# Performance work log

Hardware: AMD Instinct MI355X
Metric: run time of the kernel (lower is better)

The kernel has to match this reference:

```python
import jax, jax.numpy as jnp
import numpy as np

B, C, N, K = 1, 64, 65536, 16

def setup_inputs() -> dict:
    key = jax.random.key(0)
    ks = jax.random.split(key, 12)
    s = 0.02
    return {
        "spa": jax.random.normal(ks[0], (B, C, N), jnp.float32),
        "spe": jax.random.normal(ks[1], (B, C, N), jnp.float32),
        "neighbor_indices": jax.random.randint(ks[2], (B, N, K), 0, N, jnp.int64),
        # spa_MHA params (torch Linear weights, shape [out,in])
        "WQ_spa": jax.random.normal(ks[3], (C, C), jnp.float32) * s,
        "WK_spa": jax.random.normal(ks[4], (C, C), jnp.float32) * s,
        "WV_spa": jax.random.normal(ks[5], (C, C), jnp.float32) * s,
        "bV_spa": jnp.zeros((C,), jnp.float32),
        # spe_MHA params
        "WQ_spe": jax.random.normal(ks[6], (C, C), jnp.float32) * s,
        "WK_spe": jax.random.normal(ks[7], (C, C), jnp.float32) * s,
        "WV_spe": jax.random.normal(ks[8], (C, C), jnp.float32) * s,
        "bV_spe": jnp.zeros((C,), jnp.float32),
    }


def _cross_att(q, nb, WQ, WK, WV, bV):
    # q: [B,N,C], nb: [B,N,K,C]
    Q = jnp.einsum('bnc,dc->bnd', q, WQ)            # [B,N,C]
    Kk = jnp.einsum('bnkc,dc->bnkd', nb, WK)        # [B,N,K,C]
    V = jnp.einsum('bnkc,dc->bnkd', nb, WV) + bV    # [B,N,K,C]
    scores = jnp.einsum('bnd,bnkd->bnk', Q, Kk) / np.sqrt(Q.shape[-1]).astype(Q.dtype)
    attn = jax.nn.softmax(scores, axis=-1)          # [B,N,K]
    ctx = jnp.einsum('bnk,bnkd->bnd', attn, V)      # [B,N,C]
    return ctx.transpose(0, 2, 1)                   # [B,C,N]


def reference(spa, spe, neighbor_indices,
              WQ_spa, WK_spa, WV_spa, bV_spa,
              WQ_spe, WK_spe, WV_spe, bV_spe):
    dims = spa.shape[1]
    feature = jnp.concatenate([spa, spe], axis=1)   # [B,2C,N]
    # gather neighbors: [B,2C,N,K]
    nb = jax.vmap(lambda f, idx: f[:, idx])(feature, neighbor_indices)
    feature_q = feature.transpose(0, 2, 1)          # [B,N,2C]
    nb = nb.transpose(0, 2, 3, 1)                   # [B,N,K,2C]
    spa_feat = _cross_att(feature_q[..., :dims], nb[..., dims:],
                          WQ_spa, WK_spa, WV_spa, bV_spa)
    spe_feat = _cross_att(feature_q[..., dims:], nb[..., :dims],
                          WQ_spe, WK_spe, WV_spe, bV_spe)
    fusion = jnp.concatenate([spa_feat, spe_feat], axis=1)  # [B,2C,N]
    return feature + fusion
```

## Files before the change

kernel.cpp:

```cpp
#include <hip/hip_runtime.h>

#define NPTS 65536

__device__ __forceinline__ float bf_lo(unsigned u) { return __uint_as_float(u << 16); }
__device__ __forceinline__ float bf_hi(unsigned u) { return __uint_as_float(u & 0xFFFF0000u); }
__device__ __forceinline__ unsigned short f2bf(float f) {
    unsigned u = __float_as_uint(f);
    return (unsigned short)((u + 0x7FFFu + ((u >> 16) & 1u)) >> 16);
}
__device__ __forceinline__ float bfu(unsigned short us) {
    return __uint_as_float(((unsigned)us) << 16);
}
__device__ __forceinline__ unsigned pktrunc(float a, float b) {
    return (__float_as_uint(a) >> 16) | (__float_as_uint(b) & 0xFFFF0000u);
}
__device__ __forceinline__ void unpack8(uint4 v, float* o) {
    o[0] = bf_lo(v.x); o[1] = bf_hi(v.x); o[2] = bf_lo(v.y); o[3] = bf_hi(v.y);
    o[4] = bf_lo(v.z); o[5] = bf_hi(v.z); o[6] = bf_lo(v.w); o[7] = bf_hi(v.w);
}
#if __has_builtin(__builtin_amdgcn_fdot2_f32_bf16)
typedef __bf16 bf16x2 __attribute__((ext_vector_type(2)));
__device__ __forceinline__ float dot2acc(unsigned a, unsigned b, float c) {
    return __builtin_amdgcn_fdot2_f32_bf16(__builtin_bit_cast(bf16x2, a),
                                           __builtin_bit_cast(bf16x2, b), c, false);
}
#else
__device__ __forceinline__ float dot2acc(unsigned a, unsigned b, float c) {
    return c + bf_lo(a) * bf_lo(b) + bf_hi(a) * bf_hi(b);
}
#endif
#if __has_builtin(__builtin_amdgcn_rcpf)
__device__ __forceinline__ float fastrcp(float x) { return __builtin_amdgcn_rcpf(x); }
#else
__device__ __forceinline__ float fastrcp(float x) { return 1.0f / x; }
#endif

#if __has_builtin(__builtin_amdgcn_cvt_pk_f32_fp8) && __has_builtin(__builtin_amdgcn_cvt_pk_fp8_f32)
#define USE_FP8 1
typedef float floatx2 __attribute__((ext_vector_type(2)));
__device__ __forceinline__ void unpk_fp8_u32(unsigned u, float* o) {
    floatx2 lo = __builtin_amdgcn_cvt_pk_f32_fp8((int)u, false);
    floatx2 hi = __builtin_amdgcn_cvt_pk_f32_fp8((int)u, true);
    o[0] = lo[0]; o[1] = lo[1]; o[2] = hi[0]; o[3] = hi[1];
}
__device__ __forceinline__ unsigned pk_fp8_4(float a, float b, float c, float d) {
    int v = __builtin_amdgcn_cvt_pk_fp8_f32(a, b, 0, false);
    v = __builtin_amdgcn_cvt_pk_fp8_f32(c, d, v, true);
    return (unsigned)v;
}
#else
#define USE_FP8 0
#endif

typedef __attribute__((ext_vector_type(8))) short short8;
typedef __attribute__((ext_vector_type(4))) float f32x4;

__global__ __launch_bounds__(256) void k_matM(const float* __restrict__ WQa,
                                              const float* __restrict__ WKa,
                                              const float* __restrict__ WQe,
                                              const float* __restrict__ WKe,
                                              const float* __restrict__ WVa,
                                              const float* __restrict__ WVe,
                                              unsigned short* __restrict__ Mt,
                                              unsigned short* __restrict__ WVb) {
    const int t = threadIdx.x;
    if (blockIdx.x >= 8) {
        const int which = blockIdx.x - 8;
        const float* WV = which ? WVe : WVa;
        unsigned short* dst = WVb + which * 4096;
        #pragma unroll
        for (int i = 0; i < 16; ++i) dst[t + i * 256] = f2bf(WV[t + i * 256]);
        return;
    }
    __shared__ float WKs[4096];
    __shared__ float WQs[64][16];
    const int which = blockIdx.x >> 2;
    const int c0 = (blockIdx.x & 3) * 16;
    const float* WQ = which ? WQe : WQa;
    const float* WK = which ? WKe : WKa;
    #pragma unroll
    for (int i = 0; i < 16; ++i) WKs[t + i * 256] = WK[t + i * 256];
    #pragma unroll
    for (int i = 0; i < 4; ++i) {
        const int id = t + i * 256;
        WQs[id >> 4][id & 15] = WQ[(id >> 4) * 64 + c0 + (id & 15)];
    }
    __syncthreads();
    const int cc = t >> 4;
    const int eg = t & 15;
    float a0 = 0.f, a1 = 0.f, a2 = 0.f, a3 = 0.f;
    #pragma unroll
    for (int d = 0; d < 64; ++d) {
        const float wq = WQs[d][cc];
        const float4 wk = *reinterpret_cast<const float4*>(&WKs[d * 64 + eg * 4]);
        a0 += wq * wk.x; a1 += wq * wk.y; a2 += wq * wk.z; a3 += wq * wk.w;
    }
    const int c = c0 + cc;
    Mt[which * 4096 + (eg * 4 + 0) * 64 + c] = f2bf(a0);
    Mt[which * 4096 + (eg * 4 + 1) * 64 + c] = f2bf(a1);
    Mt[which * 4096 + (eg * 4 + 2) * 64 + c] = f2bf(a2);
    Mt[which * 4096 + (eg * 4 + 3) * 64 + c] = f2bf(a3);
}

__global__ __launch_bounds__(256) void k_prep(const float* __restrict__ spa,
                                              const float* __restrict__ spe,
                                              const unsigned short* __restrict__ Mt,
                                              unsigned short* __restrict__ featT,
                                              unsigned char* __restrict__ featQ,
                                              unsigned short* __restrict__ qeff) {
    __shared__ unsigned short tb[64][136];
    __shared__ unsigned short ml[2][64][72];
    const int n0 = blockIdx.x * 64;
    const int t = threadIdx.x;
    #pragma unroll
    for (int i = 0; i < 4; ++i) {
        const int id = t + i * 256;
        const int which = id >> 9;
        const int row = (id >> 3) & 63;
        const int q = id & 7;
        *reinterpret_cast<uint4*>(&ml[which][row][q * 8]) =
            *reinterpret_cast<const uint4*>(Mt + which * 4096 + row * 64 + q * 8);
    }
    {
        const int p = t & 63;
        const int c0 = 2 * (t >> 6);
        #pragma unroll
        for (int i = 0; i < 16; ++i) {
            const int c = c0 + 8 * i;
            const float v0 = (c < 64) ? spa[c * NPTS + n0 + p]
                                      : spe[(c - 64) * NPTS + n0 + p];
            const float v1 = (c + 1 < 64) ? spa[(c + 1) * NPTS + n0 + p]
                                          : spe[(c + 1 - 64) * NPTS + n0 + p];
            *reinterpret_cast<unsigned*>(&tb[p][c]) =
                (unsigned)f2bf(v0) | ((unsigned)f2bf(v1) << 16);
        }
    }
    __syncthreads();
    {
        const int pt = t >> 2;
        const int q = t & 3;
        const uint4* src = reinterpret_cast<const uint4*>(&tb[pt][q * 32]);
        const uint4 s0 = src[0], s1 = src[1], s2 = src[2], s3 = src[3];
        uint4* dst = reinterpret_cast<uint4*>(featT + (size_t)(n0 + pt) * 128 + q * 32);
        dst[0] = s0; dst[1] = s1; dst[2] = s2; dst[3] = s3;
#if USE_FP8
        unsigned o0 = pk_fp8_4(bf_lo(s0.x), bf_hi(s0.x), bf_lo(s0.y), bf_hi(s0.y));
        unsigned o1 = pk_fp8_4(bf_lo(s0.z), bf_hi(s0.z), bf_lo(s0.w), bf_hi(s0.w));
        unsigned o2 = pk_fp8_4(bf_lo(s1.x), bf_hi(s1.x), bf_lo(s1.y), bf_hi(s1.y));
        unsigned o3 = pk_fp8_4(bf_lo(s1.z), bf_hi(s1.z), bf_lo(s1.w), bf_hi(s1.w));
        unsigned o4 = pk_fp8_4(bf_lo(s2.x), bf_hi(s2.x), bf_lo(s2.y), bf_hi(s2.y));
        unsigned o5 = pk_fp8_4(bf_lo(s2.z), bf_hi(s2.z), bf_lo(s2.w), bf_hi(s2.w));
        unsigned o6 = pk_fp8_4(bf_lo(s3.x), bf_hi(s3.x), bf_lo(s3.y), bf_hi(s3.y));
        unsigned o7 = pk_fp8_4(bf_lo(s3.z), bf_hi(s3.z), bf_lo(s3.w), bf_hi(s3.w));
        uint4* qd = reinterpret_cast<uint4*>(featQ + (size_t)(n0 + pt) * 128 + q * 32);
        qd[0] = make_uint4(o0, o1, o2, o3);
        qd[1] = make_uint4(o4, o5, o6, o7);
#endif
    }
    const int w = t >> 6;
    const int l = t & 63;
    const int lrow = l & 15;
    const int lk8 = (l >> 4) * 8;
    short8 afr[2][2];
    #pragma unroll
    for (int half = 0; half < 2; ++half)
        #pragma unroll
        for (int kc = 0; kc < 2; ++kc)
            afr[half][kc] = __builtin_bit_cast(short8,
                *reinterpret_cast<const uint4*>(&tb[w * 16 + lrow][half * 64 + kc * 32 + lk8]));
    f32x4 acc[8];
    #pragma unroll
    for (int et = 0; et < 8; ++et) acc[et] = (f32x4){0.f, 0.f, 0.f, 0.f};
    #pragma unroll
    for (int et = 0; et < 8; ++et) {
        const int which = et >> 2;
        const int el = (et & 3) * 16 + lrow;
        #pragma unroll
        for (int kc = 0; kc < 2; ++kc) {
            const short8 bfr = __builtin_bit_cast(short8,
                *reinterpret_cast<const uint4*>(&ml[which][el][kc * 32 + lk8]));
            acc[et] = __builtin_amdgcn_mfma_f32_16x16x32_bf16(afr[which][kc], bfr, acc[et], 0, 0, 0);
        }
    }
    #pragma unroll
    for (int et = 0; et < 8; ++et) {
        #pragma unroll
        for (int r = 0; r < 4; ++r) {
            const int n = n0 + w * 16 + (l >> 4) * 4 + r;
            qeff[(size_t)n * 128 + et * 16 + lrow] = f2bf(acc[et][r]);
        }
    }
}

__global__ __launch_bounds__(256) void k_attn(const unsigned short* __restrict__ featT,
                                              const unsigned char* __restrict__ featQ,
                                              const unsigned short* __restrict__ qeff,
                                              const int* __restrict__ idx,
                                              unsigned short* __restrict__ sTb) {
    __shared__ unsigned red[4][16][68];
    const int wave = threadIdx.x >> 6;
    const int lane = threadIdx.x & 63;
    const int n = blockIdx.x * 4 + wave;
    const int k = lane >> 2;
    const int c4 = lane & 3;

    const int j = idx[n * 16 + k];
    float xa[16], xe[16];
    unsigned bxa[8], bxe[8];
#if USE_FP8
    const uint4* fq = reinterpret_cast<const uint4*>(featQ + (size_t)j * 128);
    const uint4 FA = fq[c4], FE = fq[4 + c4];
    unpk_fp8_u32(FA.x, xa);      unpk_fp8_u32(FA.y, xa + 4);
    unpk_fp8_u32(FA.z, xa + 8);  unpk_fp8_u32(FA.w, xa + 12);
    unpk_fp8_u32(FE.x, xe);      unpk_fp8_u32(FE.y, xe + 4);
    unpk_fp8_u32(FE.z, xe + 8);  unpk_fp8_u32(FE.w, xe + 12);
    #pragma unroll
    for (int i = 0; i < 8; ++i) {
        bxa[i] = pktrunc(xa[2*i], xa[2*i + 1]);
        bxe[i] = pktrunc(xe[2*i], xe[2*i + 1]);
    }
#else
    const uint4* fx = reinterpret_cast<const uint4*>(featT + (size_t)j * 128);
    const uint4 A0 = fx[2*c4],     A1 = fx[2*c4 + 1];
    const uint4 E0 = fx[8 + 2*c4], E1 = fx[8 + 2*c4 + 1];
    unpack8(A0, xa); unpack8(A1, xa + 8);
    unpack8(E0, xe); unpack8(E1, xe + 8);
    bxa[0] = A0.x; bxa[1] = A0.y; bxa[2] = A0.z; bxa[3] = A0.w;
    bxa[4] = A1.x; bxa[5] = A1.y; bxa[6] = A1.z; bxa[7] = A1.w;
    bxe[0] = E0.x; bxe[1] = E0.y; bxe[2] = E0.z; bxe[3] = E0.w;
    bxe[4] = E1.x; bxe[5] = E1.y; bxe[6] = E1.z; bxe[7] = E1.w;
#endif
    const uint4* qx = reinterpret_cast<const uint4*>(qeff + (size_t)n * 128);
    const uint4 QA0 = qx[2*c4],     QA1 = qx[2*c4 + 1];
    const uint4 QE0 = qx[8 + 2*c4], QE1 = qx[8 + 2*c4 + 1];

    float pa = 0.f, pe = 0.f;
    pa = dot2acc(QA0.x, bxe[0], pa); pa = dot2acc(QA0.y, bxe[1], pa);
    pa = dot2acc(QA0.z, bxe[2], pa); pa = dot2acc(QA0.w, bxe[3], pa);
    pa = dot2acc(QA1.x, bxe[4], pa); pa = dot2acc(QA1.y, bxe[5], pa);
    pa = dot2acc(QA1.z, bxe[6], pa); pa = dot2acc(QA1.w, bxe[7], pa);
    pe = dot2acc(QE0.x, bxa[0], pe); pe = dot2acc(QE0.y, bxa[1], pe);
    pe = dot2acc(QE0.z, bxa[2], pe); pe = dot2acc(QE0.w, bxa[3], pe);
    pe = dot2acc(QE1.x, bxa[4], pe); pe = dot2acc(QE1.y, bxa[5], pe);
    pe = dot2acc(QE1.z, bxa[6], pe); pe = dot2acc(QE1.w, bxa[7], pe);
    pa += __shfl_xor(pa, 1); pa += __shfl_xor(pa, 2);
    pe += __shfl_xor(pe, 1); pe += __shfl_xor(pe, 2);
    const float ea = __expf(pa * 0.125f);
    const float ee = __expf(pe * 0.125f);
    float da = ea, de = ee;
    #pragma unroll
    for (int m = 4; m < 64; m <<= 1) {
        da += __shfl_xor(da, m);
        de += __shfl_xor(de, m);
    }
    const float wA = ea * fastrcp(da);
    const float wB = ee * fastrcp(de);

    unsigned pA[8], pB[8];
    #pragma unroll
    for (int i = 0; i < 8; ++i) {
        pA[i] = pktrunc(wA * xe[2*i], wA * xe[2*i + 1]);
        pB[i] = pktrunc(wB * xa[2*i], wB * xa[2*i + 1]);
    }
    {
        uint4* wa4 = reinterpret_cast<uint4*>(&red[wave][k][c4 * 8]);
        wa4[0] = make_uint4(pA[0], pA[1], pA[2], pA[3]);
        wa4[1] = make_uint4(pA[4], pA[5], pA[6], pA[7]);
        uint4* wb4 = reinterpret_cast<uint4*>(&red[wave][k][32 + c4 * 8]);
        wb4[0] = make_uint4(pB[0], pB[1], pB[2], pB[3]);
        wb4[1] = make_uint4(pB[4], pB[5], pB[6], pB[7]);
    }
    asm volatile("s_waitcnt lgkmcnt(0)" ::: "memory");
    float s0 = 0.f, s1 = 0.f;
    #pragma unroll
    for (int kk = 0; kk < 16; ++kk) {
        const unsigned v = red[wave][kk][lane];
        s0 += __uint_as_float(v << 16);
        s1 += __uint_as_float(v & 0xFFFF0000u);
    }
    reinterpret_cast<unsigned*>(sTb + (size_t)n * 128)[lane] =
        (unsigned)f2bf(s0) | ((unsigned)f2bf(s1) << 16);
}

__global__ __launch_bounds__(256, 4) void k_out(const unsigned short* __restrict__ sTb,
                                                const unsigned short* __restrict__ featT,
                                                const unsigned short* __restrict__ WVb,
                                                const float* __restrict__ bVa,
                                                const float* __restrict__ bVe,
                                                float* __restrict__ out) {
    __shared__ char smem_raw[27136];
    unsigned short* stile = reinterpret_cast<unsigned short*>(smem_raw);
    unsigned short* wvl = reinterpret_cast<unsigned short*>(smem_raw + 8704);
    float* ctxT = reinterpret_cast<float*>(smem_raw);
    const int n0 = blockIdx.x * 32;
    const int t = threadIdx.x;
    const int w = t >> 6;
    const int l = t & 63;
    const int half = w >> 1;
    const int pg = w & 1;
    const int lrow = l & 15;
    const int lk8 = (l >> 4) * 8;
    unsigned short res[4][4];
    #pragma unroll
    for (int nt = 0; nt < 4; ++nt)
        #pragma unroll
        for (int r = 0; r < 4; ++r) {
            const int pt = pg * 16 + (l >> 4) * 4 + r;
            res[nt][r] = featT[(size_t)(n0 + pt) * 128 + half * 64 + nt * 16 + lrow];
        }
    #pragma unroll
    for (int i = 0; i < 2; ++i) {
        const int id = t + i * 256;
        const int pt = id >> 4;
        const int q = id & 15;
        *reinterpret_cast<uint4*>(stile + pt * 136 + q * 8) =
            *reinterpret_cast<const uint4*>(sTb + (size_t)(n0 + pt) * 128 + q * 8);
    }
    #pragma unroll
    for (int i = 0; i < 4; ++i) {
        const int id = t + i * 256;
        const int which = id >> 9;
        const int row = (id >> 3) & 63;
        const int q = id & 7;
        *reinterpret_cast<uint4*>(wvl + which * 4608 + row * 72 + q * 8) =
            *reinterpret_cast<const uint4*>(WVb + which * 4096 + row * 64 + q * 8);
    }
    __syncthreads();
    short8 afr[2];
    #pragma unroll
    for (int kc = 0; kc < 2; ++kc)
        afr[kc] = __builtin_bit_cast(short8,
            *reinterpret_cast<const uint4*>(stile + (pg * 16 + lrow) * 136 + half * 64 + kc * 32 + lk8));
    const unsigned short* wt = wvl + half * 4608;
    const float* bV = half ? bVe : bVa;
    f32x4 acc[4];
    #pragma unroll
    for (int nt = 0; nt < 4; ++nt) {
        acc[nt] = (f32x4){0.f, 0.f, 0.f, 0.f};
        #pragma unroll
        for (int kc = 0; kc < 2; ++kc) {
            const short8 bfr = __builtin_bit_cast(short8,
                *reinterpret_cast<const uint4*>(wt + (nt * 16 + lrow) * 72 + kc * 32 + lk8));
            acc[nt] = __builtin_amdgcn_mfma_f32_16x16x32_bf16(afr[kc], bfr, acc[nt], 0, 0, 0);
        }
    }
    __syncthreads();
    #pragma unroll
    for (int nt = 0; nt < 4; ++nt) {
        const int d = nt * 16 + lrow;
        const int dglob = half * 64 + d;
        const float bias = bV[d];
        #pragma unroll
        for (int r = 0; r < 4; ++r) {
            const int pt = pg * 16 + (l >> 4) * 4 + r;
            ctxT[dglob * 33 + pt] = acc[nt][r] + bias + bfu(res[nt][r]);
        }
    }
    __syncthreads();
    {
        const int p = t & 31;
        const int ch0 = t >> 5;
        #pragma unroll
        for (int i = 0; i < 16; ++i) {
            const int ch = ch0 + (i << 3);
            out[(size_t)ch * NPTS + n0 + p] = ctxT[ch * 33 + p];
        }
    }
}

extern "C" void kernel_launch(void* const* d_in, const int* in_sizes, int n_in,
                              void* d_out, int out_size, void* d_ws, size_t ws_size,
                              hipStream_t stream) {
    const float* spa = (const float*)d_in[0];
    const float* spe = (const float*)d_in[1];
    const int* idx   = (const int*)d_in[2];
    const float* WQa = (const float*)d_in[3];
    const float* WKa = (const float*)d_in[4];
    const float* WVa = (const float*)d_in[5];
    const float* bVa = (const float*)d_in[6];
    const float* WQe = (const float*)d_in[7];
    const float* WKe = (const float*)d_in[8];
    const float* WVe = (const float*)d_in[9];
    const float* bVe = (const float*)d_in[10];
    float* out = (float*)d_out;

    char* ws = (char*)d_ws;
    unsigned short* featT = (unsigned short*)(ws);
    unsigned short* qeff  = (unsigned short*)(ws + 16777216);
    unsigned short* sTb   = (unsigned short*)(ws + 33554432);
    unsigned short* Mt    = (unsigned short*)(ws + 50331648);
    unsigned short* WVb   = (unsigned short*)(ws + 50348032);
    unsigned char*  featQ = (unsigned char*)(ws + 50364416);

    k_matM<<<10, 256, 0, stream>>>(WQa, WKa, WQe, WKe, WVa, WVe, Mt, WVb);
    k_prep<<<1024, 256, 0, stream>>>(spa, spe, Mt, featT, featQ, qeff);
    k_attn<<<16384, 256, 0, stream>>>(featT, featQ, qeff, idx, sTb);
    k_out<<<2048, 256, 0, stream>>>(sTb, featT, WVb, bVa, bVe, out);
}
```

Measured before the change: 66.27 us.

## Fold weight-product kernel into prep and convert WV inside output kernel

Removes the separate k_matM launch. Each k_prep block now recomputes the WK^T·WQ product with MFMA from fp32 weights staged in shared memory, and k_out converts WV to bf16 itself while loading. This saves one launch and the dependency bubble between kernels. In exchange, 1024 prep blocks and 2048 out blocks each redo the small weight load, conversion and extra syncs, and k_out now makes strided scalar loads instead of vector loads.

```diff
diff --git a/kernel.cpp b/kernel.cpp
--- a/kernel.cpp
+++ b/kernel.cpp
@@ -55,72 +55,24 @@
 typedef __attribute__((ext_vector_type(8))) short short8;
 typedef __attribute__((ext_vector_type(4))) float f32x4;
 
-__global__ __launch_bounds__(256) void k_matM(const float* __restrict__ WQa,
+__global__ __launch_bounds__(256) void k_prep(const float* __restrict__ spa,
+                                              const float* __restrict__ spe,
+                                              const float* __restrict__ WQa,
                                               const float* __restrict__ WKa,
                                               const float* __restrict__ WQe,
                                               const float* __restrict__ WKe,
-                                              const float* __restrict__ WVa,
-                                              const float* __restrict__ WVe,
-                                              unsigned short* __restrict__ Mt,
-                                              unsigned short* __restrict__ WVb) {
-    const int t = threadIdx.x;
-    if (blockIdx.x >= 8) {
-        const int which = blockIdx.x - 8;
-        const float* WV = which ? WVe : WVa;
-        unsigned short* dst = WVb + which * 4096;
-        #pragma unroll
-        for (int i = 0; i < 16; ++i) dst[t + i * 256] = f2bf(WV[t + i * 256]);
-        return;
-    }
-    __shared__ float WKs[4096];
-    __shared__ float WQs[64][16];
-    const int which = blockIdx.x >> 2;
-    const int c0 = (blockIdx.x & 3) * 16;
-    const float* WQ = which ? WQe : WQa;
-    const float* WK = which ? WKe : WKa;
-    #pragma unroll
-    for (int i = 0; i < 16; ++i) WKs[t + i * 256] = WK[t + i * 256];
-    #pragma unroll
-    for (int i = 0; i < 4; ++i) {
-        const int id = t + i * 256;
-        WQs[id >> 4][id & 15] = WQ[(id >> 4) * 64 + c0 + (id & 15)];
-    }
-    __syncthreads();
-    const int cc = t >> 4;
-    const int eg = t & 15;
-    float a0 = 0.f, a1 = 0.f, a2 = 0.f, a3 = 0.f;
-    #pragma unroll
-    for (int d = 0; d < 64; ++d) {
-        const float wq = WQs[d][cc];
-        const float4 wk = *reinterpret_cast<const float4*>(&WKs[d * 64 + eg * 4]);
-        a0 += wq * wk.x; a1 += wq * wk.y; a2 += wq * wk.z; a3 += wq * wk.w;
-    }
-    const int c = c0 + cc;
-    Mt[which * 4096 + (eg * 4 + 0) * 64 + c] = f2bf(a0);
-    Mt[which * 4096 + (eg * 4 + 1) * 64 + c] = f2bf(a1);
-    Mt[which * 4096 + (eg * 4 + 2) * 64 + c] = f2bf(a2);
-    Mt[which * 4096 + (eg * 4 + 3) * 64 + c] = f2bf(a3);
-}
-
-__global__ __launch_bounds__(256) void k_prep(const float* __restrict__ spa,
-                                              const float* __restrict__ spe,
-                                              const unsigned short* __restrict__ Mt,
                                               unsigned short* __restrict__ featT,
                                               unsigned char* __restrict__ featQ,
                                               unsigned short* __restrict__ qeff) {
     __shared__ unsigned short tb[64][136];
-    __shared__ unsigned short ml[2][64][72];
+    __shared__ unsigned short msh[2][64][72];
     const int n0 = blockIdx.x * 64;
     const int t = threadIdx.x;
-    #pragma unroll
-    for (int i = 0; i < 4; ++i) {
-        const int id = t + i * 256;
-        const int which = id >> 9;
-        const int row = (id >> 3) & 63;
-        const int q = id & 7;
-        *reinterpret_cast<uint4*>(&ml[which][row][q * 8]) =
-            *reinterpret_cast<const uint4*>(Mt + which * 4096 + row * 64 + q * 8);
-    }
+    const int w = t >> 6;
+    const int l = t & 63;
+    const int lrow = l & 15;
+    const int lk8 = (l >> 4) * 8;
+
     {
         const int p = t & 63;
         const int c0 = 2 * (t >> 6);
@@ -133,6 +85,74 @@
                                           : spe[(c + 1 - 64) * NPTS + n0 + p];
             *reinterpret_cast<unsigned*>(&tb[p][c]) =
                 (unsigned)f2bf(v0) | ((unsigned)f2bf(v1) << 16);
+        }
+    }
+    unsigned short* msh0 = &msh[0][0][0];
+    unsigned short* msh1 = &msh[1][0][0];
+    f32x4 macc_a[4], macc_e[4];
+    #pragma unroll
+    for (int ct = 0; ct < 4; ++ct) {
+        macc_a[ct] = (f32x4){0.f, 0.f, 0.f, 0.f};
+        macc_e[ct] = (f32x4){0.f, 0.f, 0.f, 0.f};
+    }
+    #pragma unroll
+    for (int i = 0; i < 16; ++i) {
+        const int id = t + i * 256;
+        const int d = id >> 6;
+        const int e = id & 63;
+        msh0[e * 72 + d] = f2bf(WKa[d * 64 + e]);
+        msh1[e * 72 + d] = f2bf(WQa[d * 64 + e]);
+    }
+    __syncthreads();
+    {
+        const short8 a0 = __builtin_bit_cast(short8,
+            *reinterpret_cast<const uint4*>(msh0 + (w * 16 + lrow) * 72 + lk8));
+        const short8 a1 = __builtin_bit_cast(short8,
+            *reinterpret_cast<const uint4*>(msh0 + (w * 16 + lrow) * 72 + 32 + lk8));
+        #pragma unroll
+        for (int ct = 0; ct < 4; ++ct) {
+            const short8 b0 = __builtin_bit_cast(short8,
+                *reinterpret_cast<const uint4*>(msh1 + (ct * 16 + lrow) * 72 + lk8));
+            const short8 b1 = __builtin_bit_cast(short8,
+                *reinterpret_cast<const uint4*>(msh1 + (ct * 16 + lrow) * 72 + 32 + lk8));
+            macc_a[ct] = __builtin_amdgcn_mfma_f32_16x16x32_bf16(a0, b0, macc_a[ct], 0, 0, 0);
+            macc_a[ct] = __builtin_amdgcn_mfma_f32_16x16x32_bf16(a1, b1, macc_a[ct], 0, 0, 0);
+        }
+    }
+    __syncthreads();
+    #pragma unroll
+    for (int i = 0; i < 16; ++i) {
+        const int id = t + i * 256;
+        const int d = id >> 6;
+        const int e = id & 63;
+        msh0[e * 72 + d] = f2bf(WKe[d * 64 + e]);
+        msh1[e * 72 + d] = f2bf(WQe[d * 64 + e]);
+    }
+    __syncthreads();
+    {
+        const short8 a0 = __builtin_bit_cast(short8,
+            *reinterpret_cast<const uint4*>(msh0 + (w * 16 + lrow) * 72 + lk8));
+        const short8 a1 = __builtin_bit_cast(short8,
+            *reinterpret_cast<const uint4*>(msh0 + (w * 16 + lrow) * 72 + 32 + lk8));
+        #pragma unroll
+        for (int ct = 0; ct < 4; ++ct) {
+            const short8 b0 = __builtin_bit_cast(short8,
+                *reinterpret_cast<const uint4*>(msh1 + (ct * 16 + lrow) * 72 + lk8));
+            const short8 b1 = __builtin_bit_cast(short8,
+                *reinterpret_cast<const uint4*>(msh1 + (ct * 16 + lrow) * 72 + 32 + lk8));
+            macc_e[ct] = __builtin_amdgcn_mfma_f32_16x16x32_bf16(a0, b0, macc_e[ct], 0, 0, 0);
+            macc_e[ct] = __builtin_amdgcn_mfma_f32_16x16x32_bf16(a1, b1, macc_e[ct], 0, 0, 0);
+        }
+    }
+    __syncthreads();
+    #pragma unroll
+    for (int ct = 0; ct < 4; ++ct) {
+        #pragma unroll
+        for (int r = 0; r < 4; ++r) {
+            const int e = w * 16 + (l >> 4) * 4 + r;
+            const int c = ct * 16 + (l & 15);
+            msh0[e * 72 + c] = f2bf(macc_a[ct][r]);
+            msh1[e * 72 + c] = f2bf(macc_e[ct][r]);
         }
     }
     __syncthreads();
@@ -157,10 +177,6 @@
         qd[1] = make_uint4(o4, o5, o6, o7);
 #endif
     }
-    const int w = t >> 6;
-    const int l = t & 63;
-    const int lrow = l & 15;
-    const int lk8 = (l >> 4) * 8;
     short8 afr[2][2];
     #pragma unroll
     for (int half = 0; half < 2; ++half)
@@ -175,10 +191,11 @@
     for (int et = 0; et < 8; ++et) {
         const int which = et >> 2;
         const int el = (et & 3) * 16 + lrow;
+        const unsigned short* mlb = which ? msh1 : msh0;
         #pragma unroll
         for (int kc = 0; kc < 2; ++kc) {
             const short8 bfr = __builtin_bit_cast(short8,
-                *reinterpret_cast<const uint4*>(&ml[which][el][kc * 32 + lk8]));
+                *reinterpret_cast<const uint4*>(mlb + el * 72 + kc * 32 + lk8));
             acc[et] = __builtin_amdgcn_mfma_f32_16x16x32_bf16(afr[which][kc], bfr, acc[et], 0, 0, 0);
         }
     }
@@ -284,8 +301,9 @@
 
 __global__ __launch_bounds__(256, 4) void k_out(const unsigned short* __restrict__ sTb,
                                                 const unsigned short* __restrict__ featT,
-                                                const unsigned short* __restrict__ WVb,
+                                                const float* __restrict__ WVa,
                                                 const float* __restrict__ bVa,
+                                                const float* __restrict__ WVe,
                                                 const float* __restrict__ bVe,
                                                 float* __restrict__ out) {
     __shared__ char smem_raw[27136];
@@ -317,13 +335,12 @@
             *reinterpret_cast<const uint4*>(sTb + (size_t)(n0 + pt) * 128 + q * 8);
     }
     #pragma unroll
-    for (int i = 0; i < 4; ++i) {
-        const int id = t + i * 256;
-        const int which = id >> 9;
-        const int row = (id >> 3) & 63;
-        const int q = id & 7;
-        *reinterpret_cast<uint4*>(wvl + which * 4608 + row * 72 + q * 8) =
-            *reinterpret_cast<const uint4*>(WVb + which * 4096 + row * 64 + q * 8);
+    for (int i = 0; i < 32; ++i) {
+        const int id = t + (i << 8);
+        const int which = id >> 12;
+        const int d = (id >> 6) & 63;
+        const int e = id & 63;
+        wvl[which * 4608 + d * 72 + e] = f2bf((which ? WVe : WVa)[d * 64 + e]);
     }
     __syncthreads();
     short8 afr[2];
@@ -388,12 +405,10 @@
     unsigned short* featT = (unsigned short*)(ws);
     unsigned short* qeff  = (unsigned short*)(ws + 16777216);
     unsigned short* sTb   = (unsigned short*)(ws + 33554432);
-    unsigned short* Mt    = (unsigned short*)(ws + 50331648);
-    unsigned short* WVb   = (unsigned short*)(ws + 50348032);
-    unsigned char*  featQ = (unsigned char*)(ws + 50364416);
-
-    k_matM<<<10, 256, 0, stream>>>(WQa, WKa, WQe, WKe, WVa, WVe, Mt, WVb);
-    k_prep<<<1024, 256, 0, stream>>>(spa, spe, Mt, featT, featQ, qeff);
+    unsigned char*  featQ = (unsigned char*)(ws + 50331648);
+
+    k_prep<<<1024, 256, 0, stream>>>(spa, spe, WQa, WKa, WQe, WKe,
+                                     featT, featQ, qeff);
     k_attn<<<16384, 256, 0, stream>>>(featT, featQ, qeff, idx, sTb);
-    k_out<<<2048, 256, 0, stream>>>(sTb, featT, WVb, bVa, bVe, out);
-}
+    k_out<<<2048, 256, 0, stream>>>(sTb, featT, WVa, bVa, WVe, bVe, out);
+}
```

Result: no change. 67.06 us (+1.2%).
